# Kernel tuning notes

Measured on AMD Instinct MI355X. Metric: run time of the kernel, lower is better.

## Reference

```python
import jax, jax.numpy as jnp
import numpy as np

EMB_DIM = 512
N_HEADS = 8
HEAD_DIM = EMB_DIM // N_HEADS


def setup_inputs() -> dict:
    key = jax.random.key(0)
    k1, k2, k3, k4, k5 = jax.random.split(key, 5)
    B, S = 4, 2048
    x = jax.random.normal(k1, (B, S, EMB_DIM), dtype=jnp.float32)
    # nn.Linear params: weight [out, in], bias [out]
    W_qkv = jax.random.normal(k2, (3 * EMB_DIM, EMB_DIM), dtype=jnp.float32) * (EMB_DIM ** -0.5)
    b_qkv = jax.random.normal(k3, (3 * EMB_DIM,), dtype=jnp.float32) * 0.02
    W_out = jax.random.normal(k4, (EMB_DIM, EMB_DIM), dtype=jnp.float32) * (EMB_DIM ** -0.5)
    b_out = jax.random.normal(k5, (EMB_DIM,), dtype=jnp.float32) * 0.02
    return {"x": x, "W_qkv": W_qkv, "b_qkv": b_qkv, "W_out": W_out, "b_out": b_out}


def reference(x, W_qkv, b_qkv, W_out, b_out):
    B, S, E = x.shape
    scale = E ** (-0.5)  # note: scores are DIVIDED by this, i.e. multiplied by sqrt(E)
    qkv = x @ W_qkv.T + b_qkv                       # [B, S, 3E]
    qkv = qkv.reshape(B, S, N_HEADS, 3 * HEAD_DIM).transpose(0, 2, 1, 3)  # [B, H, S, 3d]
    q, k, v = jnp.split(qkv, 3, axis=-1)            # each [B, H, S, d]
    scores = jnp.einsum("bhqd,bhkd->bhqk", q, k) / scale
    attn = jax.nn.softmax(scores, axis=-1)
    attn = jax.nn.softmax(attn, axis=-1)            # double softmax, faithful to source
    o = jnp.einsum("bhqk,bhkd->bhqd", attn, v)      # [B, H, S, d]
    o = o.transpose(0, 2, 1, 3).reshape(B, S, E)
    return o @ W_out.T + b_out
```

## Files before the change

### kernel.cpp

```cpp
#include <hip/hip_runtime.h>

typedef __bf16 bf16;
typedef __attribute__((ext_vector_type(4))) __bf16 bf16x4;
typedef __attribute__((ext_vector_type(8))) __bf16 bf16x8;
typedef __attribute__((ext_vector_type(4))) float f32x4;

#define MFMA(A,B,C) __builtin_amdgcn_mfma_f32_16x16x32_bf16(A,B,C,0,0,0)

#define SEQ 2048
#define EMB 512
#define HD  64
#define SCALE 22.627416997969522f
#define NEG_SEED -3.0e4f

__global__ __launch_bounds__(256)
void convert_kernel(const float* __restrict__ x, const float* __restrict__ Wqkv,
                    const float* __restrict__ Wout,
                    bf16* __restrict__ Xh, bf16* __restrict__ Xl,
                    bf16* __restrict__ Wqh, bf16* __restrict__ Wql,
                    bf16* __restrict__ Wo) {
  const int NX = 8192 * 512 / 4;
  const int NW = 1536 * 512 / 4;
  const int NO = 512 * 512 / 4;
  const int stride = gridDim.x * 256;
  for (int i = blockIdx.x * 256 + threadIdx.x; i < NX + NW + NO; i += stride) {
    const float* src; bf16 *dh, *dl; int j; bool haslo;
    if (i < NX)           { src = x;    dh = Xh;  dl = Xl;  j = i;           haslo = true; }
    else if (i < NX + NW) { src = Wqkv; dh = Wqh; dl = Wql; j = i - NX;      haslo = true; }
    else                  { src = Wout; dh = Wo;  dl = Wo;  j = i - NX - NW; haslo = false; }
    f32x4 v = *(const f32x4*)&src[(size_t)j * 4];
    bf16x4 h4, l4;
#pragma unroll
    for (int r = 0; r < 4; ++r) {
      bf16 h = (bf16)v[r]; h4[r] = h; l4[r] = (bf16)(v[r] - (float)h);
    }
    *(bf16x4*)&dh[(size_t)j * 4] = h4;
    if (haslo) *(bf16x4*)&dl[(size_t)j * 4] = l4;
  }
}

__global__ __launch_bounds__(256)
void gemm_qkv(const bf16* __restrict__ Xh, const bf16* __restrict__ Xl,
              const bf16* __restrict__ Wh, const bf16* __restrict__ Wl,
              const float* __restrict__ bias,
              bf16* __restrict__ Qh, bf16* __restrict__ Ql,
              bf16* __restrict__ Kh, bf16* __restrict__ Kl,
              bf16* __restrict__ Vrm) {
  __shared__ __align__(16) bf16 Ah[64][64], Al[64][64];
  __shared__ __align__(16) bf16 Bh[64][64], Bl[64][64];
  const int tid  = threadIdx.x;
  const int lane = tid & 63, wave = tid >> 6;
  const int lin = blockIdx.x + gridDim.x * blockIdx.y;
  const int xcd = lin & 7;
  const int w_  = lin >> 3;
  const int m0 = ((w_ & 15) + xcd * 16) * 64;
  const int n0 = (w_ >> 4) * 64;
  const int wm = (wave >> 1) * 32, wn = (wave & 1) * 32;
  const int c = lane & 15, quad = lane >> 4;
  const int sr   = tid >> 3;
  const int scol = (tid & 7) * 8;
  const int sphy = ((tid & 7) ^ (sr & 7)) * 8;

  const f32x4 zero = {0.f, 0.f, 0.f, 0.f};
  f32x4 acc[2][2];
  acc[0][0] = zero; acc[0][1] = zero; acc[1][0] = zero; acc[1][1] = zero;

  for (int k0 = 0; k0 < 512; k0 += 64) {
    *(bf16x8*)&Ah[sr][sphy]      = *(const bf16x8*)&Xh[(size_t)(m0 + sr     ) * 512 + k0 + scol];
    *(bf16x8*)&Ah[sr + 32][sphy] = *(const bf16x8*)&Xh[(size_t)(m0 + sr + 32) * 512 + k0 + scol];
    *(bf16x8*)&Al[sr][sphy]      = *(const bf16x8*)&Xl[(size_t)(m0 + sr     ) * 512 + k0 + scol];
    *(bf16x8*)&Al[sr + 32][sphy] = *(const bf16x8*)&Xl[(size_t)(m0 + sr + 32) * 512 + k0 + scol];
    *(bf16x8*)&Bh[sr][sphy]      = *(const bf16x8*)&Wh[(size_t)(n0 + sr     ) * 512 + k0 + scol];
    *(bf16x8*)&Bh[sr + 32][sphy] = *(const bf16x8*)&Wh[(size_t)(n0 + sr + 32) * 512 + k0 + scol];
    *(bf16x8*)&Bl[sr][sphy]      = *(const bf16x8*)&Wl[(size_t)(n0 + sr     ) * 512 + k0 + scol];
    *(bf16x8*)&Bl[sr + 32][sphy] = *(const bf16x8*)&Wl[(size_t)(n0 + sr + 32) * 512 + k0 + scol];
    __syncthreads();
#pragma unroll
    for (int ks = 0; ks < 64; ks += 32) {
      const int px = (((ks >> 3) + quad) ^ (c & 7)) * 8;
      bf16x8 ah0 = *(bf16x8*)&Ah[wm + c     ][px];
      bf16x8 ah1 = *(bf16x8*)&Ah[wm + 16 + c][px];
      bf16x8 al0 = *(bf16x8*)&Al[wm + c     ][px];
      bf16x8 al1 = *(bf16x8*)&Al[wm + 16 + c][px];
      bf16x8 bh0 = *(bf16x8*)&Bh[wn + c     ][px];
      bf16x8 bh1 = *(bf16x8*)&Bh[wn + 16 + c][px];
      bf16x8 bl0 = *(bf16x8*)&Bl[wn + c     ][px];
      bf16x8 bl1 = *(bf16x8*)&Bl[wn + 16 + c][px];
      acc[0][0] = MFMA(ah0, bh0, acc[0][0]);
      acc[0][0] = MFMA(al0, bh0, acc[0][0]);
      acc[0][0] = MFMA(ah0, bl0, acc[0][0]);
      acc[0][1] = MFMA(ah0, bh1, acc[0][1]);
      acc[0][1] = MFMA(al0, bh1, acc[0][1]);
      acc[0][1] = MFMA(ah0, bl1, acc[0][1]);
      acc[1][0] = MFMA(ah1, bh0, acc[1][0]);
      acc[1][0] = MFMA(al1, bh0, acc[1][0]);
      acc[1][0] = MFMA(ah1, bl0, acc[1][0]);
      acc[1][1] = MFMA(ah1, bh1, acc[1][1]);
      acc[1][1] = MFMA(al1, bh1, acc[1][1]);
      acc[1][1] = MFMA(ah1, bl1, acc[1][1]);
    }
    __syncthreads();
  }

#pragma unroll
  for (int mt = 0; mt < 2; ++mt) {
#pragma unroll
    for (int nt = 0; nt < 2; ++nt) {
      const int n = n0 + wn + nt * 16 + c;
      const float bv = bias[n];
#pragma unroll
      for (int r = 0; r < 4; ++r) {
        const int m = m0 + wm + mt * 16 + quad * 4 + r;
        float v = acc[mt][nt][r] + bv;
        const int h = n / 192, t = n % 192;
        const size_t bh = (size_t)((m >> 11) * 8 + h);
        const int s = m & 2047;
        if (t < 64) {
          float q = v * SCALE;
          bf16 hi = (bf16)q;
          float lo = q - (float)hi;
          size_t idx = (bh * SEQ + s) * HD + t;
          Qh[idx] = hi; Ql[idx] = (bf16)lo;
        } else if (t < 128) {
          bf16 hi = (bf16)v;
          float lo = v - (float)hi;
          size_t idx = (bh * SEQ + s) * HD + (t - 64);
          Kh[idx] = hi; Kl[idx] = (bf16)lo;
        } else {
          Vrm[(bh * SEQ + s) * HD + (t - 128)] = (bf16)v;
        }
      }
    }
  }
}

__global__ __launch_bounds__(256)
void gemm_out(const bf16* __restrict__ A, const bf16* __restrict__ Wo,
              const float* __restrict__ bias, float* __restrict__ C) {
  __shared__ __align__(16) bf16 As[64][64];
  __shared__ __align__(16) bf16 Bs[64][64];
  const int tid  = threadIdx.x;
  const int lane = tid & 63, wave = tid >> 6;
  const int lin = blockIdx.x + gridDim.x * blockIdx.y;
  const int xcd = lin & 7;
  const int w_  = lin >> 3;
  const int m0 = ((w_ & 15) + xcd * 16) * 64;
  const int n0 = (w_ >> 4) * 64;
  const int wm = (wave >> 1) * 32, wn = (wave & 1) * 32;
  const int c = lane & 15, quad = lane >> 4;
  const int sr   = tid >> 3;
  const int scol = (tid & 7) * 8;
  const int sphy = ((tid & 7) ^ (sr & 7)) * 8;

  const f32x4 zero = {0.f, 0.f, 0.f, 0.f};
  f32x4 acc[2][2];
  acc[0][0] = zero; acc[0][1] = zero; acc[1][0] = zero; acc[1][1] = zero;

  for (int k0 = 0; k0 < 512; k0 += 64) {
    *(bf16x8*)&As[sr][sphy]      = *(const bf16x8*)&A [(size_t)(m0 + sr     ) * 512 + k0 + scol];
    *(bf16x8*)&As[sr + 32][sphy] = *(const bf16x8*)&A [(size_t)(m0 + sr + 32) * 512 + k0 + scol];
    *(bf16x8*)&Bs[sr][sphy]      = *(const bf16x8*)&Wo[(size_t)(n0 + sr     ) * 512 + k0 + scol];
    *(bf16x8*)&Bs[sr + 32][sphy] = *(const bf16x8*)&Wo[(size_t)(n0 + sr + 32) * 512 + k0 + scol];
    __syncthreads();
#pragma unroll
    for (int ks = 0; ks < 64; ks += 32) {
      const int px = (((ks >> 3) + quad) ^ (c & 7)) * 8;
      bf16x8 a0 = *(bf16x8*)&As[wm + c     ][px];
      bf16x8 a1 = *(bf16x8*)&As[wm + 16 + c][px];
      bf16x8 b0 = *(bf16x8*)&Bs[wn + c     ][px];
      bf16x8 b1 = *(bf16x8*)&Bs[wn + 16 + c][px];
      acc[0][0] = MFMA(a0, b0, acc[0][0]);
      acc[0][1] = MFMA(a0, b1, acc[0][1]);
      acc[1][0] = MFMA(a1, b0, acc[1][0]);
      acc[1][1] = MFMA(a1, b1, acc[1][1]);
    }
    __syncthreads();
  }

#pragma unroll
  for (int mt = 0; mt < 2; ++mt) {
#pragma unroll
    for (int nt = 0; nt < 2; ++nt) {
      const int n = n0 + wn + nt * 16 + c;
      const float bv = bias[n];
#pragma unroll
      for (int r = 0; r < 4; ++r) {
        const int m = m0 + wm + mt * 16 + quad * 4 + r;
        C[(size_t)m * 512 + n] = acc[mt][nt][r] + bv;
      }
    }
  }
}

__global__ __launch_bounds__(256)
void vsum_kernel(const bf16* __restrict__ Vrm, float* __restrict__ Vp) {
  __shared__ float red[32][64];
  const int pc = blockIdx.x >> 5;
  const int bh = blockIdx.x & 31;
  const bf16* p = Vrm + ((size_t)bh * SEQ + pc * 256) * HD;
  const int g  = threadIdx.x >> 3;
  const int dc = (threadIdx.x & 7) * 8;
  float s[8] = {0.f,0.f,0.f,0.f,0.f,0.f,0.f,0.f};
  for (int s0 = g; s0 < 256; s0 += 32) {
    bf16x8 v = *(const bf16x8*)&p[(size_t)s0 * HD + dc];
#pragma unroll
    for (int j = 0; j < 8; ++j) s[j] += (float)v[j];
  }
#pragma unroll
  for (int j = 0; j < 8; ++j) red[g][dc + j] = s[j];
  __syncthreads();
  if (threadIdx.x < 64) {
    float a = 0.f;
#pragma unroll
    for (int g2 = 0; g2 < 32; ++g2) a += red[g2][threadIdx.x];
    Vp[(size_t)(pc * 32 + bh) * 64 + threadIdx.x] = a;
  }
}

__global__ __launch_bounds__(512, 4)
void attn_kernel(const bf16* __restrict__ Qh, const bf16* __restrict__ Ql,
                 const bf16* __restrict__ Kh, const bf16* __restrict__ Kl,
                 const bf16* __restrict__ Vrm, const float* __restrict__ Vp,
                 bf16* __restrict__ O) {
  __shared__ __align__(16) char pool[32768];
  __shared__ unsigned char cms8[8][128][16];
  __shared__ float plistP[8][16][16];
  __shared__ unsigned short plistI[8][16][16];
  __shared__ int pcnt[8][16];
  bf16 (*SK)[64] = (bf16(*)[64])pool;

  const int tid  = threadIdx.x;
  const int lane = tid & 63, wave = tid >> 6;
  const int c = lane & 15, quad = lane >> 4;
  const int bh = blockIdx.x;
  const int q0 = blockIdx.y * 128 + wave * 16;
  const size_t hoff = (size_t)bh * SEQ * HD;
  const bf16* qh_p = Qh + hoff;
  const bf16* ql_p = Ql + hoff;
  const bf16* kh_p = Kh + hoff;
  const bf16* kl_p = Kl + hoff;
  const bf16* v_p  = Vrm + hoff;
  const f32x4 zero = {0.f, 0.f, 0.f, 0.f};

  const int sr   = tid >> 3;
  const int scol = (tid & 7) * 8;
  const int sphy = ((tid & 7) ^ (sr & 7)) * 8;
  const int pc0  = ((0 + quad) ^ (c & 7)) * 8;
  const int pc1  = ((4 + quad) ^ (c & 7)) * 8;

  bf16x8 qf[2], qlf[2];
#pragma unroll
  for (int t = 0; t < 2; ++t) {
    size_t off = (size_t)(q0 + c) * HD + t * 32 + quad * 8;
    qf[t]  = *(const bf16x8*)&qh_p[off];
    qlf[t] = *(const bf16x8*)&ql_p[off];
  }

  bf16x8 pA = *(const bf16x8*)&kh_p[(size_t)sr * HD + scol];
  bf16x8 pB = *(const bf16x8*)&kh_p[(size_t)(sr + 64) * HD + scol];
  *(bf16x8*)&SK[sr][sphy]      = pA;
  *(bf16x8*)&SK[sr + 64][sphy] = pB;
  __syncthreads();
  int buf = 0;
  float mqL = NEG_SEED;
  for (int cs = 0; cs < 16; ++cs) {
    if (cs < 15) {
      const size_t k0 = (size_t)(cs + 1) * 128;
      pA = *(const bf16x8*)&kh_p[(k0 + sr) * HD + scol];
      pB = *(const bf16x8*)&kh_p[(k0 + sr + 64) * HD + scol];
    }
#pragma unroll
    for (int t = 0; t < 8; ++t) {
      bf16x8 k0 = *(bf16x8*)&SK[buf * 128 + t * 16 + c][pc0];
      bf16x8 k1 = *(bf16x8*)&SK[buf * 128 + t * 16 + c][pc1];
      f32x4 sc = MFMA(k0, qf[0], zero);
      sc = MFMA(k1, qf[1], sc);
      float cm = fmaxf(fmaxf(sc[0], sc[1]), fmaxf(sc[2], sc[3]));
      mqL = fmaxf(mqL, cm);
      float c2 = fmaxf(cm, __shfl_xor(cm, 16, 64));
      c2 = fmaxf(c2, __shfl_xor(c2, 32, 64));
      if (quad == 0) {
        int qv = (int)(c2 * 0.125f + 128.5f);
        qv = qv < 0 ? 0 : (qv > 255 ? 255 : qv);
        cms8[wave][cs * 8 + t][c] = (unsigned char)qv;
      }
    }
    if (cs < 15) {
      const int nb = buf ^ 1;
      *(bf16x8*)&SK[nb * 128 + sr][sphy]      = pA;
      *(bf16x8*)&SK[nb * 128 + sr + 64][sphy] = pB;
      __syncthreads();
      buf = nb;
    }
  }
  __syncthreads();
  float mq = fmaxf(mqL, __shfl_xor(mqL, 16, 64));
  mq = fmaxf(mq, __shfl_xor(mq, 32, 64));

  if (lane < 16) pcnt[wave][lane] = 0;
  pA = *(const bf16x8*)&kh_p[(size_t)sr * HD + scol];
  pB = *(const bf16x8*)&kh_p[(size_t)(sr + 64) * HD + scol];
  *(bf16x8*)&SK[sr][sphy]      = pA;
  *(bf16x8*)&SK[sr + 64][sphy] = pB;
  __syncthreads();
  buf = 0;
  float l1 = 0.f;
  for (int cb = 0; cb < 16; ++cb) {
    if (cb < 15) {
      const size_t k0 = (size_t)(cb + 1) * 128;
      pA = *(const bf16x8*)&kh_p[(k0 + sr) * HD + scol];
      pB = *(const bf16x8*)&kh_p[(k0 + sr + 64) * HD + scol];
    }
#pragma unroll
    for (int t = 0; t < 8; ++t) {
      const int g = cb * 8 + t;
      const float cv = (float)((int)cms8[wave][g][c] - 128) * 8.0f;
      if (__any(cv > mq - 28.f)) {
        bf16x8 kh0 = *(bf16x8*)&SK[buf * 128 + t * 16 + c][pc0];
        bf16x8 kh1 = *(bf16x8*)&SK[buf * 128 + t * 16 + c][pc1];
        const size_t krow = (size_t)(g * 16 + c) * HD;
        bf16x8 kl0 = *(const bf16x8*)&kl_p[krow + quad * 8];
        bf16x8 kl1 = *(const bf16x8*)&kl_p[krow + 32 + quad * 8];
        f32x4 sc = MFMA(kh0, qf[0], zero);
        sc = MFMA(kh0, qlf[0], sc);
        sc = MFMA(kh1, qf[1],  sc);
        sc = MFMA(kh1, qlf[1], sc);
        sc = MFMA(kl0, qf[0],  sc);
        sc = MFMA(kl1, qf[1],  sc);
#pragma unroll
        for (int r = 0; r < 4; ++r) {
          const float d = sc[r] - mq;
          const float p = __expf(d);
          l1 += p;
          if (d > -16.f) {
            const int slot = atomicAdd(&pcnt[wave][c], 1);
            if (slot < 16) {
              plistP[wave][c][slot] = p;
              plistI[wave][c][slot] = (unsigned short)(g * 16 + quad * 4 + r);
            }
          }
        }
      }
    }
    if (cb < 15) {
      const int nb = buf ^ 1;
      *(bf16x8*)&SK[nb * 128 + sr][sphy]      = pA;
      *(bf16x8*)&SK[nb * 128 + sr + 64][sphy] = pB;
      __syncthreads();
      buf = nb;
    }
  }
  l1 += __shfl_xor(l1, 16, 64);
  l1 += __shfl_xor(l1, 32, 64);

  const float inv1 = 1.f / l1;
  float oc[16];
#pragma unroll
  for (int i = 0; i < 16; ++i) oc[i] = 0.f;
  float l2 = 0.f;
  const int n = min(pcnt[wave][c], 16);
  for (int j = 0; j < n; ++j) {
    const float a1 = plistP[wave][c][j] * inv1;
    const int  idx = plistI[wave][c][j];
    const float t1 = __expf(a1) - 1.0f;
    l2 += t1;
    const bf16* vp = &v_p[(size_t)idx * HD + quad * 4];
#pragma unroll
    for (int dt = 0; dt < 4; ++dt) {
      bf16x4 v4 = *(const bf16x4*)&vp[dt * 16];
#pragma unroll
      for (int r = 0; r < 4; ++r) oc[dt * 4 + r] += t1 * (float)v4[r];
    }
  }

  const int b = bh >> 3, h = bh & 7;
  const float rcp = 1.f / (2048.f + l2);
  const float* vpp = Vp + (size_t)bh * HD;
  bf16* orow = &O[((size_t)b * SEQ + q0 + c) * EMB + h * HD];
#pragma unroll
  for (int dt = 0; dt < 4; ++dt) {
    f32x4 vt4 = zero;
#pragma unroll
    for (int pc = 0; pc < 8; ++pc)
      vt4 += *(const f32x4*)&vpp[(size_t)pc * 32 * 64 + dt * 16 + quad * 4];
    bf16x4 ov;
#pragma unroll
    for (int r = 0; r < 4; ++r) ov[r] = (bf16)((oc[dt * 4 + r] + vt4[r]) * rcp);
    *(bf16x4*)&orow[dt * 16 + quad * 4] = ov;
  }
}

extern "C" void kernel_launch(void* const* d_in, const int* in_sizes, int n_in,
                              void* d_out, int out_size, void* d_ws, size_t ws_size,
                              hipStream_t stream) {
  const float* x    = (const float*)d_in[0];
  const float* Wqkv = (const float*)d_in[1];
  const float* bqkv = (const float*)d_in[2];
  const float* Wout = (const float*)d_in[3];
  const float* bout = (const float*)d_in[4];
  float* out = (float*)d_out;

  char* ws = (char*)d_ws;
  const size_t SZ = (size_t)32 * SEQ * HD * 2;
  bf16* Qh  = (bf16*)(ws + 0 * SZ);
  bf16* Ql  = (bf16*)(ws + 1 * SZ);
  bf16* Kh  = (bf16*)(ws + 2 * SZ);
  bf16* Kl  = (bf16*)(ws + 3 * SZ);
  bf16* Vrm = (bf16*)(ws + 4 * SZ);
  bf16* XhO = (bf16*)(ws + 5 * SZ);
  bf16* Xl  = (bf16*)(ws + 6 * SZ);
  bf16* Wqh = (bf16*)(ws + 7 * SZ);
  bf16* Wql = (bf16*)(ws + 7 * SZ + 0x180000);
  bf16* Wo  = (bf16*)(ws + 7 * SZ + 0x300000);
  float* Vp = (float*)(ws + 7 * SZ + 0x380000);

  convert_kernel<<<dim3(2048), 256, 0, stream>>>(x, Wqkv, Wout, XhO, Xl, Wqh, Wql, Wo);
  gemm_qkv<<<dim3(128, 24), 256, 0, stream>>>(XhO, Xl, Wqh, Wql, bqkv, Qh, Ql, Kh, Kl, Vrm);
  vsum_kernel<<<dim3(256), 256, 0, stream>>>(Vrm, Vp);
  attn_kernel<<<dim3(32, SEQ / 128), 512, 0, stream>>>(Qh, Ql, Kh, Kl, Vrm, Vp, XhO);
  gemm_out<<<dim3(128, 8), 256, 0, stream>>>(XhO, Wo, bout, out);
}
```

Measured before the change: 214.3 us.

## Gather active key tiles via ballot and skip lo-precision terms for V

In the QKV GEMM, output tiles that belong to V now use only the high bf16 halves, dropping the split-precision correction MFMAs and the lo loads. V is stored only as bf16, so those corrections are treated as wasted work. The attention second pass first builds a per-wave bitmask of key tiles that pass the threshold, using the quantized chunk maxima and ballots. It then walks only those tiles, loading K hi/lo straight from global memory with two-deep register prefetching. This replaces the block-wide shared-memory staging of all 16 chunks and its barriers, and the barrier after pass one is dropped. The cost is less reuse of K across waves and more global traffic per wave, plus slightly lower precision for V.

```diff
diff --git a/kernel.cpp b/kernel.cpp
--- a/kernel.cpp
+++ b/kernel.cpp
@@ -55,6 +55,7 @@
   const int w_  = lin >> 3;
   const int m0 = ((w_ & 15) + xcd * 16) * 64;
   const int n0 = (w_ >> 4) * 64;
+  const bool isV = ((n0 % 192) == 128);
   const int wm = (wave >> 1) * 32, wn = (wave & 1) * 32;
   const int c = lane & 15, quad = lane >> 4;
   const int sr   = tid >> 3;
@@ -68,36 +69,45 @@
   for (int k0 = 0; k0 < 512; k0 += 64) {
     *(bf16x8*)&Ah[sr][sphy]      = *(const bf16x8*)&Xh[(size_t)(m0 + sr     ) * 512 + k0 + scol];
     *(bf16x8*)&Ah[sr + 32][sphy] = *(const bf16x8*)&Xh[(size_t)(m0 + sr + 32) * 512 + k0 + scol];
-    *(bf16x8*)&Al[sr][sphy]      = *(const bf16x8*)&Xl[(size_t)(m0 + sr     ) * 512 + k0 + scol];
-    *(bf16x8*)&Al[sr + 32][sphy] = *(const bf16x8*)&Xl[(size_t)(m0 + sr + 32) * 512 + k0 + scol];
     *(bf16x8*)&Bh[sr][sphy]      = *(const bf16x8*)&Wh[(size_t)(n0 + sr     ) * 512 + k0 + scol];
     *(bf16x8*)&Bh[sr + 32][sphy] = *(const bf16x8*)&Wh[(size_t)(n0 + sr + 32) * 512 + k0 + scol];
-    *(bf16x8*)&Bl[sr][sphy]      = *(const bf16x8*)&Wl[(size_t)(n0 + sr     ) * 512 + k0 + scol];
-    *(bf16x8*)&Bl[sr + 32][sphy] = *(const bf16x8*)&Wl[(size_t)(n0 + sr + 32) * 512 + k0 + scol];
+    if (!isV) {
+      *(bf16x8*)&Al[sr][sphy]      = *(const bf16x8*)&Xl[(size_t)(m0 + sr     ) * 512 + k0 + scol];
+      *(bf16x8*)&Al[sr + 32][sphy] = *(const bf16x8*)&Xl[(size_t)(m0 + sr + 32) * 512 + k0 + scol];
+      *(bf16x8*)&Bl[sr][sphy]      = *(const bf16x8*)&Wl[(size_t)(n0 + sr     ) * 512 + k0 + scol];
+      *(bf16x8*)&Bl[sr + 32][sphy] = *(const bf16x8*)&Wl[(size_t)(n0 + sr + 32) * 512 + k0 + scol];
+    }
     __syncthreads();
 #pragma unroll
     for (int ks = 0; ks < 64; ks += 32) {
       const int px = (((ks >> 3) + quad) ^ (c & 7)) * 8;
       bf16x8 ah0 = *(bf16x8*)&Ah[wm + c     ][px];
       bf16x8 ah1 = *(bf16x8*)&Ah[wm + 16 + c][px];
-      bf16x8 al0 = *(bf16x8*)&Al[wm + c     ][px];
-      bf16x8 al1 = *(bf16x8*)&Al[wm + 16 + c][px];
       bf16x8 bh0 = *(bf16x8*)&Bh[wn + c     ][px];
       bf16x8 bh1 = *(bf16x8*)&Bh[wn + 16 + c][px];
-      bf16x8 bl0 = *(bf16x8*)&Bl[wn + c     ][px];
-      bf16x8 bl1 = *(bf16x8*)&Bl[wn + 16 + c][px];
-      acc[0][0] = MFMA(ah0, bh0, acc[0][0]);
-      acc[0][0] = MFMA(al0, bh0, acc[0][0]);
-      acc[0][0] = MFMA(ah0, bl0, acc[0][0]);
-      acc[0][1] = MFMA(ah0, bh1, acc[0][1]);
-      acc[0][1] = MFMA(al0, bh1, acc[0][1]);
-      acc[0][1] = MFMA(ah0, bl1, acc[0][1]);
-      acc[1][0] = MFMA(ah1, bh0, acc[1][0]);
-      acc[1][0] = MFMA(al1, bh0, acc[1][0]);
-      acc[1][0] = MFMA(ah1, bl0, acc[1][0]);
-      acc[1][1] = MFMA(ah1, bh1, acc[1][1]);
-      acc[1][1] = MFMA(al1, bh1, acc[1][1]);
-      acc[1][1] = MFMA(ah1, bl1, acc[1][1]);
+      if (isV) {
+        acc[0][0] = MFMA(ah0, bh0, acc[0][0]);
+        acc[0][1] = MFMA(ah0, bh1, acc[0][1]);
+        acc[1][0] = MFMA(ah1, bh0, acc[1][0]);
+        acc[1][1] = MFMA(ah1, bh1, acc[1][1]);
+      } else {
+        bf16x8 al0 = *(bf16x8*)&Al[wm + c     ][px];
+        bf16x8 al1 = *(bf16x8*)&Al[wm + 16 + c][px];
+        bf16x8 bl0 = *(bf16x8*)&Bl[wn + c     ][px];
+        bf16x8 bl1 = *(bf16x8*)&Bl[wn + 16 + c][px];
+        acc[0][0] = MFMA(ah0, bh0, acc[0][0]);
+        acc[0][0] = MFMA(al0, bh0, acc[0][0]);
+        acc[0][0] = MFMA(ah0, bl0, acc[0][0]);
+        acc[0][1] = MFMA(ah0, bh1, acc[0][1]);
+        acc[0][1] = MFMA(al0, bh1, acc[0][1]);
+        acc[0][1] = MFMA(ah0, bl1, acc[0][1]);
+        acc[1][0] = MFMA(ah1, bh0, acc[1][0]);
+        acc[1][0] = MFMA(al1, bh0, acc[1][0]);
+        acc[1][0] = MFMA(ah1, bl0, acc[1][0]);
+        acc[1][1] = MFMA(ah1, bh1, acc[1][1]);
+        acc[1][1] = MFMA(al1, bh1, acc[1][1]);
+        acc[1][1] = MFMA(ah1, bl1, acc[1][1]);
+      }
     }
     __syncthreads();
   }
@@ -227,6 +237,7 @@
   __shared__ float plistP[8][16][16];
   __shared__ unsigned short plistI[8][16][16];
   __shared__ int pcnt[8][16];
+  __shared__ float mqs[8][16];
   bf16 (*SK)[64] = (bf16(*)[64])pool;
 
   const int tid  = threadIdx.x;
@@ -293,61 +304,68 @@
       buf = nb;
     }
   }
-  __syncthreads();
   float mq = fmaxf(mqL, __shfl_xor(mqL, 16, 64));
   mq = fmaxf(mq, __shfl_xor(mq, 32, 64));
 
+  if (quad == 0) mqs[wave][c] = mq;
   if (lane < 16) pcnt[wave][lane] = 0;
-  pA = *(const bf16x8*)&kh_p[(size_t)sr * HD + scol];
-  pB = *(const bf16x8*)&kh_p[(size_t)(sr + 64) * HD + scol];
-  *(bf16x8*)&SK[sr][sphy]      = pA;
-  *(bf16x8*)&SK[sr + 64][sphy] = pB;
-  __syncthreads();
-  buf = 0;
+  bool pr0 = false, pr1 = false;
+#pragma unroll
+  for (int cc = 0; cc < 16; ++cc) {
+    const float th = mqs[wave][cc] - 28.f;
+    pr0 |= ((float)((int)cms8[wave][lane     ][cc] - 128) * 8.0f) > th;
+    pr1 |= ((float)((int)cms8[wave][lane + 64][cc] - 128) * 8.0f) > th;
+  }
+  unsigned long long a0 = __ballot(pr0);
+  unsigned long long a1 = __ballot(pr1);
+
   float l1 = 0.f;
-  for (int cb = 0; cb < 16; ++cb) {
-    if (cb < 15) {
-      const size_t k0 = (size_t)(cb + 1) * 128;
-      pA = *(const bf16x8*)&kh_p[(k0 + sr) * HD + scol];
-      pB = *(const bf16x8*)&kh_p[(k0 + sr + 64) * HD + scol];
-    }
-#pragma unroll
-    for (int t = 0; t < 8; ++t) {
-      const int g = cb * 8 + t;
-      const float cv = (float)((int)cms8[wave][g][c] - 128) * 8.0f;
-      if (__any(cv > mq - 28.f)) {
-        bf16x8 kh0 = *(bf16x8*)&SK[buf * 128 + t * 16 + c][pc0];
-        bf16x8 kh1 = *(bf16x8*)&SK[buf * 128 + t * 16 + c][pc1];
-        const size_t krow = (size_t)(g * 16 + c) * HD;
-        bf16x8 kl0 = *(const bf16x8*)&kl_p[krow + quad * 8];
-        bf16x8 kl1 = *(const bf16x8*)&kl_p[krow + 32 + quad * 8];
-        f32x4 sc = MFMA(kh0, qf[0], zero);
-        sc = MFMA(kh0, qlf[0], sc);
-        sc = MFMA(kh1, qf[1],  sc);
-        sc = MFMA(kh1, qlf[1], sc);
-        sc = MFMA(kl0, qf[0],  sc);
-        sc = MFMA(kl1, qf[1],  sc);
-#pragma unroll
-        for (int r = 0; r < 4; ++r) {
-          const float d = sc[r] - mq;
-          const float p = __expf(d);
-          l1 += p;
-          if (d > -16.f) {
-            const int slot = atomicAdd(&pcnt[wave][c], 1);
-            if (slot < 16) {
-              plistP[wave][c][slot] = p;
-              plistI[wave][c][slot] = (unsigned short)(g * 16 + quad * 4 + r);
-            }
-          }
-        }
-      }
-    }
-    if (cb < 15) {
-      const int nb = buf ^ 1;
-      *(bf16x8*)&SK[nb * 128 + sr][sphy]      = pA;
-      *(bf16x8*)&SK[nb * 128 + sr + 64][sphy] = pB;
-      __syncthreads();
-      buf = nb;
+
+#define POPG(dst) do { \
+    if (a0) { dst = __builtin_ctzll(a0); a0 &= a0 - 1; } \
+    else if (a1) { dst = 64 + __builtin_ctzll(a1); a1 &= a1 - 1; } \
+    else dst = -1; } while (0)
+
+#define LOADK(g, K0, K1, K2, K3) do { \
+    const size_t kr_ = (size_t)((g) * 16 + c) * HD + quad * 8; \
+    K0 = *(const bf16x8*)&kh_p[kr_]; \
+    K1 = *(const bf16x8*)&kh_p[kr_ + 32]; \
+    K2 = *(const bf16x8*)&kl_p[kr_]; \
+    K3 = *(const bf16x8*)&kl_p[kr_ + 32]; } while (0)
+
+#define PROC_TILE(g, K0, K1, K2, K3) do { \
+    f32x4 sc_ = MFMA(K0, qf[0], zero); \
+    sc_ = MFMA(K0, qlf[0], sc_); \
+    sc_ = MFMA(K1, qf[1],  sc_); \
+    sc_ = MFMA(K1, qlf[1], sc_); \
+    sc_ = MFMA(K2, qf[0],  sc_); \
+    sc_ = MFMA(K3, qf[1],  sc_); \
+    for (int r_ = 0; r_ < 4; ++r_) { \
+      const float d_ = sc_[r_] - mq; \
+      const float p_ = __expf(d_); \
+      l1 += p_; \
+      if (d_ > -16.f) { \
+        const int slot_ = atomicAdd(&pcnt[wave][c], 1); \
+        if (slot_ < 16) { \
+          plistP[wave][c][slot_] = p_; \
+          plistI[wave][c][slot_] = (unsigned short)((g) * 16 + quad * 4 + r_); \
+        } \
+      } \
+    } } while (0)
+
+  {
+    int gA, gB;
+    bf16x8 A0{}, A1{}, A2{}, A3{}, B0{}, B1{}, B2{}, B3{};
+    POPG(gA);
+    if (gA >= 0) LOADK(gA, A0, A1, A2, A3);
+    while (gA >= 0) {
+      POPG(gB);
+      if (gB >= 0) LOADK(gB, B0, B1, B2, B3);
+      PROC_TILE(gA, A0, A1, A2, A3);
+      if (gB < 0) break;
+      POPG(gA);
+      if (gA >= 0) LOADK(gA, A0, A1, A2, A3);
+      PROC_TILE(gB, B0, B1, B2, B3);
     }
   }
   l1 += __shfl_xor(l1, 16, 64);
@@ -360,9 +378,9 @@
   float l2 = 0.f;
   const int n = min(pcnt[wave][c], 16);
   for (int j = 0; j < n; ++j) {
-    const float a1 = plistP[wave][c][j] * inv1;
+    const float a1v = plistP[wave][c][j] * inv1;
     const int  idx = plistI[wave][c][j];
-    const float t1 = __expf(a1) - 1.0f;
+    const float t1 = __expf(a1v) - 1.0f;
     l2 += t1;
     const bf16* vp = &v_p[(size_t)idx * HD + quad * 4];
 #pragma unroll
```

Result: no change. 218.6 us (+2.0%).

## Single-pass online max in attention, fuse V column sums into QKV GEMM

Applied to the files above, without the earlier changes.

The attention kernel drops its separate max-estimation pass over K and uses an online running max with rescaling of l1, storing raw scores in the candidate list. V column sums are now computed in the QKV GEMM epilogue with atomics into a buffer zeroed by the convert kernel, which removes the vsum kernel launch. V tiles use plain bf16 GEMM without the hi/lo split correction terms. Attention blocks shrink to 256 threads covering 64 queries, and each thread loads four K rows per stage.

```diff
diff --git a/kernel.cpp b/kernel.cpp
--- a/kernel.cpp
+++ b/kernel.cpp
@@ -18,7 +18,8 @@
                     const float* __restrict__ Wout,
                     bf16* __restrict__ Xh, bf16* __restrict__ Xl,
                     bf16* __restrict__ Wqh, bf16* __restrict__ Wql,
-                    bf16* __restrict__ Wo) {
+                    bf16* __restrict__ Wo, float* __restrict__ Vs) {
+  if (blockIdx.x < 8) Vs[blockIdx.x * 256 + threadIdx.x] = 0.f;
   const int NX = 8192 * 512 / 4;
   const int NW = 1536 * 512 / 4;
   const int NO = 512 * 512 / 4;
@@ -45,7 +46,7 @@
               const float* __restrict__ bias,
               bf16* __restrict__ Qh, bf16* __restrict__ Ql,
               bf16* __restrict__ Kh, bf16* __restrict__ Kl,
-              bf16* __restrict__ Vrm) {
+              bf16* __restrict__ Vrm, float* __restrict__ Vs) {
   __shared__ __align__(16) bf16 Ah[64][64], Al[64][64];
   __shared__ __align__(16) bf16 Bh[64][64], Bl[64][64];
   const int tid  = threadIdx.x;
@@ -55,6 +56,7 @@
   const int w_  = lin >> 3;
   const int m0 = ((w_ & 15) + xcd * 16) * 64;
   const int n0 = (w_ >> 4) * 64;
+  const bool isV = ((n0 % 192) == 128);
   const int wm = (wave >> 1) * 32, wn = (wave & 1) * 32;
   const int c = lane & 15, quad = lane >> 4;
   const int sr   = tid >> 3;
@@ -68,66 +70,97 @@
   for (int k0 = 0; k0 < 512; k0 += 64) {
     *(bf16x8*)&Ah[sr][sphy]      = *(const bf16x8*)&Xh[(size_t)(m0 + sr     ) * 512 + k0 + scol];
     *(bf16x8*)&Ah[sr + 32][sphy] = *(const bf16x8*)&Xh[(size_t)(m0 + sr + 32) * 512 + k0 + scol];
-    *(bf16x8*)&Al[sr][sphy]      = *(const bf16x8*)&Xl[(size_t)(m0 + sr     ) * 512 + k0 + scol];
-    *(bf16x8*)&Al[sr + 32][sphy] = *(const bf16x8*)&Xl[(size_t)(m0 + sr + 32) * 512 + k0 + scol];
     *(bf16x8*)&Bh[sr][sphy]      = *(const bf16x8*)&Wh[(size_t)(n0 + sr     ) * 512 + k0 + scol];
     *(bf16x8*)&Bh[sr + 32][sphy] = *(const bf16x8*)&Wh[(size_t)(n0 + sr + 32) * 512 + k0 + scol];
-    *(bf16x8*)&Bl[sr][sphy]      = *(const bf16x8*)&Wl[(size_t)(n0 + sr     ) * 512 + k0 + scol];
-    *(bf16x8*)&Bl[sr + 32][sphy] = *(const bf16x8*)&Wl[(size_t)(n0 + sr + 32) * 512 + k0 + scol];
+    if (!isV) {
+      *(bf16x8*)&Al[sr][sphy]      = *(const bf16x8*)&Xl[(size_t)(m0 + sr     ) * 512 + k0 + scol];
+      *(bf16x8*)&Al[sr + 32][sphy] = *(const bf16x8*)&Xl[(size_t)(m0 + sr + 32) * 512 + k0 + scol];
+      *(bf16x8*)&Bl[sr][sphy]      = *(const bf16x8*)&Wl[(size_t)(n0 + sr     ) * 512 + k0 + scol];
+      *(bf16x8*)&Bl[sr + 32][sphy] = *(const bf16x8*)&Wl[(size_t)(n0 + sr + 32) * 512 + k0 + scol];
+    }
     __syncthreads();
 #pragma unroll
     for (int ks = 0; ks < 64; ks += 32) {
       const int px = (((ks >> 3) + quad) ^ (c & 7)) * 8;
       bf16x8 ah0 = *(bf16x8*)&Ah[wm + c     ][px];
       bf16x8 ah1 = *(bf16x8*)&Ah[wm + 16 + c][px];
-      bf16x8 al0 = *(bf16x8*)&Al[wm + c     ][px];
-      bf16x8 al1 = *(bf16x8*)&Al[wm + 16 + c][px];
       bf16x8 bh0 = *(bf16x8*)&Bh[wn + c     ][px];
       bf16x8 bh1 = *(bf16x8*)&Bh[wn + 16 + c][px];
-      bf16x8 bl0 = *(bf16x8*)&Bl[wn + c     ][px];
-      bf16x8 bl1 = *(bf16x8*)&Bl[wn + 16 + c][px];
-      acc[0][0] = MFMA(ah0, bh0, acc[0][0]);
-      acc[0][0] = MFMA(al0, bh0, acc[0][0]);
-      acc[0][0] = MFMA(ah0, bl0, acc[0][0]);
-      acc[0][1] = MFMA(ah0, bh1, acc[0][1]);
-      acc[0][1] = MFMA(al0, bh1, acc[0][1]);
-      acc[0][1] = MFMA(ah0, bl1, acc[0][1]);
-      acc[1][0] = MFMA(ah1, bh0, acc[1][0]);
-      acc[1][0] = MFMA(al1, bh0, acc[1][0]);
-      acc[1][0] = MFMA(ah1, bl0, acc[1][0]);
-      acc[1][1] = MFMA(ah1, bh1, acc[1][1]);
-      acc[1][1] = MFMA(al1, bh1, acc[1][1]);
-      acc[1][1] = MFMA(ah1, bl1, acc[1][1]);
+      if (isV) {
+        acc[0][0] = MFMA(ah0, bh0, acc[0][0]);
+        acc[0][1] = MFMA(ah0, bh1, acc[0][1]);
+        acc[1][0] = MFMA(ah1, bh0, acc[1][0]);
+        acc[1][1] = MFMA(ah1, bh1, acc[1][1]);
+      } else {
+        bf16x8 al0 = *(bf16x8*)&Al[wm + c     ][px];
+        bf16x8 al1 = *(bf16x8*)&Al[wm + 16 + c][px];
+        bf16x8 bl0 = *(bf16x8*)&Bl[wn + c     ][px];
+        bf16x8 bl1 = *(bf16x8*)&Bl[wn + 16 + c][px];
+        acc[0][0] = MFMA(ah0, bh0, acc[0][0]);
+        acc[0][0] = MFMA(al0, bh0, acc[0][0]);
+        acc[0][0] = MFMA(ah0, bl0, acc[0][0]);
+        acc[0][1] = MFMA(ah0, bh1, acc[0][1]);
+        acc[0][1] = MFMA(al0, bh1, acc[0][1]);
+        acc[0][1] = MFMA(ah0, bl1, acc[0][1]);
+        acc[1][0] = MFMA(ah1, bh0, acc[1][0]);
+        acc[1][0] = MFMA(al1, bh0, acc[1][0]);
+        acc[1][0] = MFMA(ah1, bl0, acc[1][0]);
+        acc[1][1] = MFMA(ah1, bh1, acc[1][1]);
+        acc[1][1] = MFMA(al1, bh1, acc[1][1]);
+        acc[1][1] = MFMA(ah1, bl1, acc[1][1]);
+      }
     }
     __syncthreads();
   }
 
-#pragma unroll
-  for (int mt = 0; mt < 2; ++mt) {
+  if (isV) {
 #pragma unroll
     for (int nt = 0; nt < 2; ++nt) {
       const int n = n0 + wn + nt * 16 + c;
       const float bv = bias[n];
-#pragma unroll
-      for (int r = 0; r < 4; ++r) {
-        const int m = m0 + wm + mt * 16 + quad * 4 + r;
-        float v = acc[mt][nt][r] + bv;
-        const int h = n / 192, t = n % 192;
-        const size_t bh = (size_t)((m >> 11) * 8 + h);
-        const int s = m & 2047;
-        if (t < 64) {
-          float q = v * SCALE;
-          bf16 hi = (bf16)q;
-          float lo = q - (float)hi;
-          size_t idx = (bh * SEQ + s) * HD + t;
-          Qh[idx] = hi; Ql[idx] = (bf16)lo;
-        } else if (t < 128) {
-          bf16 hi = (bf16)v;
-          float lo = v - (float)hi;
-          size_t idx = (bh * SEQ + s) * HD + (t - 64);
-          Kh[idx] = hi; Kl[idx] = (bf16)lo;
-        } else {
-          Vrm[(bh * SEQ + s) * HD + (t - 128)] = (bf16)v;
+      const int h = n / 192, d = n % 192 - 128;
+      const size_t bh = (size_t)((m0 >> 11) * 8 + h);
+      float csum = 0.f;
+#pragma unroll
+      for (int mt = 0; mt < 2; ++mt)
+#pragma unroll
+        for (int r = 0; r < 4; ++r) {
+          const int m = m0 + wm + mt * 16 + quad * 4 + r;
+          const int s = m & 2047;
+          float v = acc[mt][nt][r] + bv;
+          Vrm[(bh * SEQ + s) * HD + d] = (bf16)v;
+          csum += v;
+        }
+      csum += __shfl_xor(csum, 16, 64);
+      csum += __shfl_xor(csum, 32, 64);
+      if (quad == 0) atomicAdd(&Vs[bh * HD + d], csum);
+    }
+  } else {
+#pragma unroll
+    for (int mt = 0; mt < 2; ++mt) {
+#pragma unroll
+      for (int nt = 0; nt < 2; ++nt) {
+        const int n = n0 + wn + nt * 16 + c;
+        const float bv = bias[n];
+#pragma unroll
+        for (int r = 0; r < 4; ++r) {
+          const int m = m0 + wm + mt * 16 + quad * 4 + r;
+          float v = acc[mt][nt][r] + bv;
+          const int h = n / 192, t = n % 192;
+          const size_t bh = (size_t)((m >> 11) * 8 + h);
+          const int s = m & 2047;
+          if (t < 64) {
+            float q = v * SCALE;
+            bf16 hi = (bf16)q;
+            float lo = q - (float)hi;
+            size_t idx = (bh * SEQ + s) * HD + t;
+            Qh[idx] = hi; Ql[idx] = (bf16)lo;
+          } else {
+            bf16 hi = (bf16)v;
+            float lo = v - (float)hi;
+            size_t idx = (bh * SEQ + s) * HD + (t - 64);
+            Kh[idx] = hi; Kl[idx] = (bf16)lo;
+          }
         }
       }
     }
@@ -192,48 +225,21 @@
   }
 }
 
-__global__ __launch_bounds__(256)
-void vsum_kernel(const bf16* __restrict__ Vrm, float* __restrict__ Vp) {
-  __shared__ float red[32][64];
-  const int pc = blockIdx.x >> 5;
-  const int bh = blockIdx.x & 31;
-  const bf16* p = Vrm + ((size_t)bh * SEQ + pc * 256) * HD;
-  const int g  = threadIdx.x >> 3;
-  const int dc = (threadIdx.x & 7) * 8;
-  float s[8] = {0.f,0.f,0.f,0.f,0.f,0.f,0.f,0.f};
-  for (int s0 = g; s0 < 256; s0 += 32) {
-    bf16x8 v = *(const bf16x8*)&p[(size_t)s0 * HD + dc];
-#pragma unroll
-    for (int j = 0; j < 8; ++j) s[j] += (float)v[j];
-  }
-#pragma unroll
-  for (int j = 0; j < 8; ++j) red[g][dc + j] = s[j];
-  __syncthreads();
-  if (threadIdx.x < 64) {
-    float a = 0.f;
-#pragma unroll
-    for (int g2 = 0; g2 < 32; ++g2) a += red[g2][threadIdx.x];
-    Vp[(size_t)(pc * 32 + bh) * 64 + threadIdx.x] = a;
-  }
-}
-
-__global__ __launch_bounds__(512, 4)
+__global__ __launch_bounds__(256, 4)
 void attn_kernel(const bf16* __restrict__ Qh, const bf16* __restrict__ Ql,
                  const bf16* __restrict__ Kh, const bf16* __restrict__ Kl,
-                 const bf16* __restrict__ Vrm, const float* __restrict__ Vp,
+                 const bf16* __restrict__ Vrm, const float* __restrict__ Vs,
                  bf16* __restrict__ O) {
-  __shared__ __align__(16) char pool[32768];
-  __shared__ unsigned char cms8[8][128][16];
-  __shared__ float plistP[8][16][16];
-  __shared__ unsigned short plistI[8][16][16];
-  __shared__ int pcnt[8][16];
-  bf16 (*SK)[64] = (bf16(*)[64])pool;
+  __shared__ __align__(16) bf16 SK[2][128][64];
+  __shared__ float plistS[4][16][16];
+  __shared__ unsigned short plistI[4][16][16];
+  __shared__ int pcnt[4][16];
 
   const int tid  = threadIdx.x;
   const int lane = tid & 63, wave = tid >> 6;
   const int c = lane & 15, quad = lane >> 4;
   const int bh = blockIdx.x;
-  const int q0 = blockIdx.y * 128 + wave * 16;
+  const int q0 = blockIdx.y * 64 + wave * 16;
   const size_t hoff = (size_t)bh * SEQ * HD;
   const bf16* qh_p = Qh + hoff;
   const bf16* ql_p = Ql + hoff;
@@ -255,97 +261,71 @@
     qf[t]  = *(const bf16x8*)&qh_p[off];
     qlf[t] = *(const bf16x8*)&ql_p[off];
   }
-
-  bf16x8 pA = *(const bf16x8*)&kh_p[(size_t)sr * HD + scol];
-  bf16x8 pB = *(const bf16x8*)&kh_p[(size_t)(sr + 64) * HD + scol];
-  *(bf16x8*)&SK[sr][sphy]      = pA;
-  *(bf16x8*)&SK[sr + 64][sphy] = pB;
+  if (lane < 16) pcnt[wave][lane] = 0;
+
+  bf16x8 pA = *(const bf16x8*)&kh_p[(size_t)(sr     ) * HD + scol];
+  bf16x8 pB = *(const bf16x8*)&kh_p[(size_t)(sr + 32) * HD + scol];
+  bf16x8 pC = *(const bf16x8*)&kh_p[(size_t)(sr + 64) * HD + scol];
+  bf16x8 pD = *(const bf16x8*)&kh_p[(size_t)(sr + 96) * HD + scol];
+  *(bf16x8*)&SK[0][sr     ][sphy] = pA;
+  *(bf16x8*)&SK[0][sr + 32][sphy] = pB;
+  *(bf16x8*)&SK[0][sr + 64][sphy] = pC;
+  *(bf16x8*)&SK[0][sr + 96][sphy] = pD;
   __syncthreads();
+
+  float mq = NEG_SEED, l1 = 0.f;
   int buf = 0;
-  float mqL = NEG_SEED;
   for (int cs = 0; cs < 16; ++cs) {
     if (cs < 15) {
       const size_t k0 = (size_t)(cs + 1) * 128;
-      pA = *(const bf16x8*)&kh_p[(k0 + sr) * HD + scol];
-      pB = *(const bf16x8*)&kh_p[(k0 + sr + 64) * HD + scol];
+      pA = *(const bf16x8*)&kh_p[(k0 + sr     ) * HD + scol];
+      pB = *(const bf16x8*)&kh_p[(k0 + sr + 32) * HD + scol];
+      pC = *(const bf16x8*)&kh_p[(k0 + sr + 64) * HD + scol];
+      pD = *(const bf16x8*)&kh_p[(k0 + sr + 96) * HD + scol];
     }
 #pragma unroll
     for (int t = 0; t < 8; ++t) {
-      bf16x8 k0 = *(bf16x8*)&SK[buf * 128 + t * 16 + c][pc0];
-      bf16x8 k1 = *(bf16x8*)&SK[buf * 128 + t * 16 + c][pc1];
-      f32x4 sc = MFMA(k0, qf[0], zero);
-      sc = MFMA(k1, qf[1], sc);
-      float cm = fmaxf(fmaxf(sc[0], sc[1]), fmaxf(sc[2], sc[3]));
-      mqL = fmaxf(mqL, cm);
-      float c2 = fmaxf(cm, __shfl_xor(cm, 16, 64));
-      c2 = fmaxf(c2, __shfl_xor(c2, 32, 64));
-      if (quad == 0) {
-        int qv = (int)(c2 * 0.125f + 128.5f);
-        qv = qv < 0 ? 0 : (qv > 255 ? 255 : qv);
-        cms8[wave][cs * 8 + t][c] = (unsigned char)qv;
-      }
-    }
-    if (cs < 15) {
-      const int nb = buf ^ 1;
-      *(bf16x8*)&SK[nb * 128 + sr][sphy]      = pA;
-      *(bf16x8*)&SK[nb * 128 + sr + 64][sphy] = pB;
-      __syncthreads();
-      buf = nb;
-    }
-  }
-  __syncthreads();
-  float mq = fmaxf(mqL, __shfl_xor(mqL, 16, 64));
-  mq = fmaxf(mq, __shfl_xor(mq, 32, 64));
-
-  if (lane < 16) pcnt[wave][lane] = 0;
-  pA = *(const bf16x8*)&kh_p[(size_t)sr * HD + scol];
-  pB = *(const bf16x8*)&kh_p[(size_t)(sr + 64) * HD + scol];
-  *(bf16x8*)&SK[sr][sphy]      = pA;
-  *(bf16x8*)&SK[sr + 64][sphy] = pB;
-  __syncthreads();
-  buf = 0;
-  float l1 = 0.f;
-  for (int cb = 0; cb < 16; ++cb) {
-    if (cb < 15) {
-      const size_t k0 = (size_t)(cb + 1) * 128;
-      pA = *(const bf16x8*)&kh_p[(k0 + sr) * HD + scol];
-      pB = *(const bf16x8*)&kh_p[(k0 + sr + 64) * HD + scol];
-    }
-#pragma unroll
-    for (int t = 0; t < 8; ++t) {
-      const int g = cb * 8 + t;
-      const float cv = (float)((int)cms8[wave][g][c] - 128) * 8.0f;
-      if (__any(cv > mq - 28.f)) {
-        bf16x8 kh0 = *(bf16x8*)&SK[buf * 128 + t * 16 + c][pc0];
-        bf16x8 kh1 = *(bf16x8*)&SK[buf * 128 + t * 16 + c][pc1];
-        const size_t krow = (size_t)(g * 16 + c) * HD;
-        bf16x8 kl0 = *(const bf16x8*)&kl_p[krow + quad * 8];
-        bf16x8 kl1 = *(const bf16x8*)&kl_p[krow + 32 + quad * 8];
-        f32x4 sc = MFMA(kh0, qf[0], zero);
+      const int g = cs * 8 + t;
+      bf16x8 kh0 = *(bf16x8*)&SK[buf][t * 16 + c][pc0];
+      bf16x8 kh1 = *(bf16x8*)&SK[buf][t * 16 + c][pc1];
+      f32x4 sc = MFMA(kh0, qf[0], zero);
+      sc = MFMA(kh1, qf[1], sc);
+      const float tm = fmaxf(fmaxf(sc[0], sc[1]), fmaxf(sc[2], sc[3]));
+      if (__any(tm > mq - 31.f)) {
+        const size_t kr = (size_t)(g * 16 + c) * HD + quad * 8;
+        bf16x8 kl0 = *(const bf16x8*)&kl_p[kr];
+        bf16x8 kl1 = *(const bf16x8*)&kl_p[kr + 32];
         sc = MFMA(kh0, qlf[0], sc);
-        sc = MFMA(kh1, qf[1],  sc);
         sc = MFMA(kh1, qlf[1], sc);
         sc = MFMA(kl0, qf[0],  sc);
         sc = MFMA(kl1, qf[1],  sc);
+        float tme = fmaxf(fmaxf(sc[0], sc[1]), fmaxf(sc[2], sc[3]));
+        tme = fmaxf(tme, __shfl_xor(tme, 16, 64));
+        tme = fmaxf(tme, __shfl_xor(tme, 32, 64));
+        if (tme > mq) {
+          l1 *= __expf(mq - tme);
+          mq = tme;
+        }
 #pragma unroll
         for (int r = 0; r < 4; ++r) {
           const float d = sc[r] - mq;
-          const float p = __expf(d);
-          l1 += p;
+          l1 += __expf(d);
           if (d > -16.f) {
             const int slot = atomicAdd(&pcnt[wave][c], 1);
             if (slot < 16) {
-              plistP[wave][c][slot] = p;
+              plistS[wave][c][slot] = sc[r];
               plistI[wave][c][slot] = (unsigned short)(g * 16 + quad * 4 + r);
             }
           }
         }
       }
     }
-    if (cb < 15) {
+    if (cs < 15) {
       const int nb = buf ^ 1;
-      *(bf16x8*)&SK[nb * 128 + sr][sphy]      = pA;
-      *(bf16x8*)&SK[nb * 128 + sr + 64][sphy] = pB;
+      *(bf16x8*)&SK[nb][sr     ][sphy] = pA;
+      *(bf16x8*)&SK[nb][sr + 32][sphy] = pB;
+      *(bf16x8*)&SK[nb][sr + 64][sphy] = pC;
+      *(bf16x8*)&SK[nb][sr + 96][sphy] = pD;
       __syncthreads();
       buf = nb;
     }
@@ -360,9 +340,10 @@
   float l2 = 0.f;
   const int n = min(pcnt[wave][c], 16);
   for (int j = 0; j < n; ++j) {
-    const float a1 = plistP[wave][c][j] * inv1;
+    const float sv = plistS[wave][c][j];
     const int  idx = plistI[wave][c][j];
-    const float t1 = __expf(a1) - 1.0f;
+    const float a1v = __expf(sv - mq) * inv1;
+    const float t1 = __expf(a1v) - 1.0f;
     l2 += t1;
     const bf16* vp = &v_p[(size_t)idx * HD + quad * 4];
 #pragma unroll
@@ -375,14 +356,11 @@
 
   const int b = bh >> 3, h = bh & 7;
   const float rcp = 1.f / (2048.f + l2);
-  const float* vpp = Vp + (size_t)bh * HD;
+  const float* vsp = Vs + bh * HD;
   bf16* orow = &O[((size_t)b * SEQ + q0 + c) * EMB + h * HD];
 #pragma unroll
   for (int dt = 0; dt < 4; ++dt) {
-    f32x4 vt4 = zero;
-#pragma unroll
-    for (int pc = 0; pc < 8; ++pc)
-      vt4 += *(const f32x4*)&vpp[(size_t)pc * 32 * 64 + dt * 16 + quad * 4];
+    f32x4 vt4 = *(const f32x4*)&vsp[dt * 16 + quad * 4];
     bf16x4 ov;
 #pragma unroll
     for (int r = 0; r < 4; ++r) ov[r] = (bf16)((oc[dt * 4 + r] + vt4[r]) * rcp);
@@ -412,11 +390,10 @@
   bf16* Wqh = (bf16*)(ws + 7 * SZ);
   bf16* Wql = (bf16*)(ws + 7 * SZ + 0x180000);
   bf16* Wo  = (bf16*)(ws + 7 * SZ + 0x300000);
-  float* Vp = (float*)(ws + 7 * SZ + 0x380000);
-
-  convert_kernel<<<dim3(2048), 256, 0, stream>>>(x, Wqkv, Wout, XhO, Xl, Wqh, Wql, Wo);
-  gemm_qkv<<<dim3(128, 24), 256, 0, stream>>>(XhO, Xl, Wqh, Wql, bqkv, Qh, Ql, Kh, Kl, Vrm);
-  vsum_kernel<<<dim3(256), 256, 0, stream>>>(Vrm, Vp);
-  attn_kernel<<<dim3(32, SEQ / 128), 512, 0, stream>>>(Qh, Ql, Kh, Kl, Vrm, Vp, XhO);
+  float* Vs = (float*)(ws + 7 * SZ + 0x380000);
+
+  convert_kernel<<<dim3(2048), 256, 0, stream>>>(x, Wqkv, Wout, XhO, Xl, Wqh, Wql, Wo, Vs);
+  gemm_qkv<<<dim3(128, 24), 256, 0, stream>>>(XhO, Xl, Wqh, Wql, bqkv, Qh, Ql, Kh, Kl, Vrm, Vs);
+  attn_kernel<<<dim3(32, 32), 256, 0, stream>>>(Qh, Ql, Kh, Kl, Vrm, Vs, XhO);
   gemm_out<<<dim3(128, 8), 256, 0, stream>>>(XhO, Wo, bout, out);
 }
```

Result: no change. 217.1 us (+1.3%).
